# Performance work log

Measured on AMD Instinct MI355X. Metric: run time of the kernel, lower is better.

## Reference

```python
import jax, jax.numpy as jnp
import numpy as np

EMBED_DIM = 64
NUM_HEADS = 8
D_K = EMBED_DIM // NUM_HEADS  # 8
B, S = 8, 1024


def setup_inputs() -> dict:
    key = jax.random.key(0)
    ks = jax.random.split(key, 10)
    f32 = jnp.float32
    lim = 1.0 / np.sqrt(EMBED_DIM)
    def lin(k):
        kw, kb = jax.random.split(k)
        w = jax.random.uniform(kw, (EMBED_DIM, EMBED_DIM), f32, -lim, lim)
        b = jax.random.uniform(kb, (EMBED_DIM,), f32, -lim, lim)
        return w, b
    wq, bq = lin(ks[0])
    wk, bk = lin(ks[1])
    wv, bv = lin(ks[2])
    wo, bo = lin(ks[3])
    theta = jax.random.normal(ks[4], (EMBED_DIM,), f32)  # trainable RY angles, one per wire
    x = jax.random.normal(ks[5], (B, S, EMBED_DIM), f32)
    return {"x": x, "wq": wq, "bq": bq, "wk": wk, "bk": bk,
            "wv": wv, "bv": bv, "theta": theta, "wo": wo, "bo": bo}


def _quantum_map(t, theta):
    # Per-qubit circuit on |0>: RX(t_i) encode, RY(theta_i), <PauliZ_i>.
    # Product state => <Z_i> = cos(theta_i) * cos(t_i) exactly.
    return jnp.cos(theta) * jnp.cos(t.reshape(-1, EMBED_DIM))  # [N, E]


def reference(x, wq, bq, wk, bk, wv, bv, theta, wo, bo):
    # Linear QKV (torch nn.Linear: x @ W^T + b)
    q = x @ wq.T + bq
    k = x @ wk.T + bk
    v = x @ wv.T + bv
    # Quantum measurement map, flattened over batch*seq (as in the original)
    q_q = _quantum_map(q, theta)  # [N, E], N = B*S
    k_q = _quantum_map(k, theta)
    v_q = _quantum_map(v, theta)
    # Full flattened attention: [N, N] scores (original never reshapes back)
    scores = (q_q @ k_q.T) / jnp.sqrt(jnp.asarray(D_K, x.dtype))
    attn = jax.nn.softmax(scores, axis=-1)  # dropout is identity in eval
    out = attn @ v_q  # [N, E]
    return out @ wo.T + bo
```

## Files before the change

### kernel.cpp

```cpp
#include <hip/hip_runtime.h>
#include <hip/hip_bf16.h>

#define NQ 8192
#define DIM 64
#define SPLITS 8
#define QBLK 128
#define BN 64
#define KEYS_PER_SPLIT (NQ / SPLITS)
#define NTILES (KEYS_PER_SPLIT / BN)
#define SCALE 0.35355339059327373f

#define KSTR 72
#define PSTR 72

typedef short s8v __attribute__((ext_vector_type(8)));
typedef float f4v __attribute__((ext_vector_type(4)));

__device__ __forceinline__ float b2f(short s) {
  unsigned int u = ((unsigned int)(unsigned short)s) << 16;
  return __uint_as_float(u);
}
__device__ __forceinline__ short f2b(float f) {
  __hip_bfloat16 h = __float2bfloat16(f);
  return *reinterpret_cast<short*>(&h);
}

#define QROWS 16
__global__ __launch_bounds__(256) void qkv_kernel(
    const float* __restrict__ x,
    const float* __restrict__ wq, const float* __restrict__ bq,
    const float* __restrict__ wk, const float* __restrict__ bk,
    const float* __restrict__ wv, const float* __restrict__ bv,
    const float* __restrict__ theta,
    short* __restrict__ qq, short* __restrict__ kq, short* __restrict__ vq) {
  __shared__ float wsh[3][DIM][DIM + 1];
  __shared__ float xs[QROWS][DIM];
  int tid = threadIdx.x;
  for (int i = tid; i < 3 * DIM * (DIM / 4); i += 256) {
    int m = i / (DIM * DIM / 4);
    int rem = i % (DIM * DIM / 4);
    int r = rem / (DIM / 4);
    int c4 = (rem % (DIM / 4)) * 4;
    const float* src = (m == 0) ? wq : (m == 1) ? wk : wv;
    float4 v = *(const float4*)&src[r * DIM + c4];
    wsh[m][r][c4 + 0] = v.x; wsh[m][r][c4 + 1] = v.y;
    wsh[m][r][c4 + 2] = v.z; wsh[m][r][c4 + 3] = v.w;
  }
  int rowbase = blockIdx.x * QROWS;
  for (int i = tid; i < QROWS * (DIM / 4); i += 256) {
    int r = i / (DIM / 4), c4 = (i % (DIM / 4)) * 4;
    float4 v = *(const float4*)&x[(rowbase + r) * DIM + c4];
    xs[r][c4 + 0] = v.x; xs[r][c4 + 1] = v.y;
    xs[r][c4 + 2] = v.z; xs[r][c4 + 3] = v.w;
  }
  __syncthreads();
  int e = tid & 63, rg = tid >> 6;
  float ct = __cosf(theta[e]);
  float bqv = bq[e], bkv = bk[e], bvv = bv[e];
  for (int r = rg; r < QROWS; r += 4) {
    float aq = bqv, ak = bkv, av = bvv;
#pragma unroll
    for (int d = 0; d < DIM; ++d) {
      float xv = xs[r][d];
      aq += xv * wsh[0][e][d];
      ak += xv * wsh[1][e][d];
      av += xv * wsh[2][e][d];
    }
    int n = rowbase + r;
    qq[n * DIM + e] = f2b(ct * __cosf(aq));
    kq[n * DIM + e] = f2b(ct * __cosf(ak));
    vq[n * DIM + e] = f2b(ct * __cosf(av));
  }
}

__global__ __launch_bounds__(256, 2) void flash_kernel(
    const short* __restrict__ qq, const short* __restrict__ kq,
    const short* __restrict__ vq,
    float* __restrict__ pO, float* __restrict__ pL) {
  __shared__ __align__(16) short ksh[BN * KSTR];
  __shared__ __align__(16) short vsh[DIM * BN];
  __shared__ __align__(16) short psh[4][32 * PSTR];

  int tid = threadIdx.x;
  int wave = tid >> 6, lane = tid & 63;
  int l15 = lane & 15, quad = lane >> 4;
  int qblock = blockIdx.x >> 3, split = blockIdx.x & 7;
  int qbase = qblock * QBLK + wave * 32;

  s8v qf[2][2];
#pragma unroll
  for (int qt = 0; qt < 2; ++qt) {
    const short* qr = qq + (qbase + qt * 16 + l15) * DIM + quad * 8;
    qf[qt][0] = *(const s8v*)qr;
    qf[qt][1] = *(const s8v*)(qr + 32);
  }

  f4v o[2][4];
  float ls[2][4];
#pragma unroll
  for (int qt = 0; qt < 2; ++qt)
#pragma unroll
    for (int c = 0; c < 4; ++c) {
      o[qt][c] = (f4v){0.f, 0.f, 0.f, 0.f};
      ls[qt][c] = 0.f;
    }

  int kstart = split * KEYS_PER_SPLIT;
  for (int t = 0; t < NTILES; ++t) {
    int kbase = kstart + t * BN;
    __syncthreads();
    for (int i = tid; i < 512; i += 256) {
      int key = i >> 3, c8 = (i & 7) << 3;
      *(s8v*)&ksh[key * KSTR + c8] = *(const s8v*)&kq[(kbase + key) * DIM + c8];
    }
    for (int i = tid; i < 512; i += 256) {
      int key = i >> 3, d0 = (i & 7) << 3;
      s8v v = *(const s8v*)&vq[(kbase + key) * DIM + d0];
      int kb = key >> 3, ko = key & 7;
#pragma unroll
      for (int j = 0; j < 8; ++j) {
        int d = d0 + j;
        vsh[d * BN + (((kb ^ ((d ^ (d >> 3)) & 7)) << 3) + ko)] = v[j];
      }
    }
    __syncthreads();

    f4v s[2][4];
#pragma unroll
    for (int n = 0; n < 4; ++n) {
      s8v kf0 = *(const s8v*)&ksh[(n * 16 + l15) * KSTR + quad * 8];
      s8v kf1 = *(const s8v*)&ksh[(n * 16 + l15) * KSTR + 32 + quad * 8];
#pragma unroll
      for (int qt = 0; qt < 2; ++qt) {
        f4v acc = {0.f, 0.f, 0.f, 0.f};
        acc = __builtin_amdgcn_mfma_f32_16x16x32_bf16(qf[qt][0], kf0, acc, 0, 0, 0);
        acc = __builtin_amdgcn_mfma_f32_16x16x32_bf16(qf[qt][1], kf1, acc, 0, 0, 0);
        s[qt][n] = acc;
      }
    }

#pragma unroll
    for (int qt = 0; qt < 2; ++qt)
#pragma unroll
      for (int n = 0; n < 4; ++n)
#pragma unroll
        for (int r = 0; r < 4; ++r) {
          float p = __expf(s[qt][n][r] * SCALE);
          short pb = f2b(p);
          ls[qt][r] += b2f(pb);
          psh[wave][(qt * 16 + quad * 4 + r) * PSTR + n * 16 + l15] = pb;
        }
    __syncthreads();

    s8v pf[2][2];
#pragma unroll
    for (int qt = 0; qt < 2; ++qt) {
      pf[qt][0] = *(const s8v*)&psh[wave][(qt * 16 + l15) * PSTR + quad * 8];
      pf[qt][1] = *(const s8v*)&psh[wave][(qt * 16 + l15) * PSTR + 32 + quad * 8];
    }
#pragma unroll
    for (int c = 0; c < 4; ++c) {
      int d = c * 16 + l15;
      int sw = (d ^ (d >> 3)) & 7;
      s8v vf0 = *(const s8v*)&vsh[d * BN + ((quad ^ sw) << 3)];
      s8v vf1 = *(const s8v*)&vsh[d * BN + (((4 + quad) ^ sw) << 3)];
#pragma unroll
      for (int qt = 0; qt < 2; ++qt) {
        o[qt][c] = __builtin_amdgcn_mfma_f32_16x16x32_bf16(pf[qt][0], vf0, o[qt][c], 0, 0, 0);
        o[qt][c] = __builtin_amdgcn_mfma_f32_16x16x32_bf16(pf[qt][1], vf1, o[qt][c], 0, 0, 0);
      }
    }
  }

#pragma unroll
  for (int qt = 0; qt < 2; ++qt)
#pragma unroll
    for (int r = 0; r < 4; ++r) {
      float v = ls[qt][r];
      v += __shfl_xor(v, 1);
      v += __shfl_xor(v, 2);
      v += __shfl_xor(v, 4);
      v += __shfl_xor(v, 8);
      ls[qt][r] = v;
    }

#pragma unroll
  for (int qt = 0; qt < 2; ++qt)
#pragma unroll
    for (int r = 0; r < 4; ++r) {
      int q = qbase + qt * 16 + quad * 4 + r;
#pragma unroll
      for (int c = 0; c < 4; ++c)
        pO[((size_t)split * NQ + q) * DIM + c * 16 + l15] = o[qt][c][r];
      if (l15 == 0) pL[split * NQ + q] = ls[qt][r];
    }
}

#define MROWS 4
__global__ __launch_bounds__(256) void merge_kernel(
    const float* __restrict__ pO, const float* __restrict__ pL,
    const float* __restrict__ wo, const float* __restrict__ bo,
    float* __restrict__ out) {
  __shared__ float wsh[DIM][DIM + 1];
  __shared__ float att[MROWS][DIM];
  int tid = threadIdx.x;
  for (int i = tid; i < DIM * (DIM / 4); i += 256) {
    int r = i / (DIM / 4), c4 = (i % (DIM / 4)) * 4;
    float4 v = *(const float4*)&wo[r * DIM + c4];
    wsh[r][c4 + 0] = v.x; wsh[r][c4 + 1] = v.y;
    wsh[r][c4 + 2] = v.z; wsh[r][c4 + 3] = v.w;
  }
  int e = tid & 63, rg = tid >> 6;
  int q = blockIdx.x * MROWS + rg;
  float s = 0.f;
#pragma unroll
  for (int sp = 0; sp < SPLITS; ++sp) s += pO[((size_t)sp * NQ + q) * DIM + e];
  float l = 0.f;
#pragma unroll
  for (int sp = 0; sp < SPLITS; ++sp) l += pL[sp * NQ + q];
  att[rg][e] = s / l;
  __syncthreads();
  float acc = bo[e];
#pragma unroll
  for (int d = 0; d < DIM; ++d) acc += att[rg][d] * wsh[e][d];
  out[q * DIM + e] = acc;
}

extern "C" void kernel_launch(void* const* d_in, const int* in_sizes, int n_in,
                              void* d_out, int out_size, void* d_ws, size_t ws_size,
                              hipStream_t stream) {
  const float* x  = (const float*)d_in[0];
  const float* wq = (const float*)d_in[1];
  const float* bq = (const float*)d_in[2];
  const float* wk = (const float*)d_in[3];
  const float* bk = (const float*)d_in[4];
  const float* wv = (const float*)d_in[5];
  const float* bv = (const float*)d_in[6];
  const float* th = (const float*)d_in[7];
  const float* wo = (const float*)d_in[8];
  const float* bo = (const float*)d_in[9];

  char* ws = (char*)d_ws;
  short* qq = (short*)(ws);
  short* kq = (short*)(ws + (1u << 20));
  short* vq = (short*)(ws + (2u << 20));
  float* pO = (float*)(ws + (3u << 20));
  float* pL = (float*)(ws + (3u << 20) + (size_t)SPLITS * NQ * DIM * 4);

  hipLaunchKernelGGL(qkv_kernel, dim3(NQ / QROWS), dim3(256), 0, stream,
                     x, wq, bq, wk, bk, wv, bv, th, qq, kq, vq);
  hipLaunchKernelGGL(flash_kernel, dim3((NQ / QBLK) * SPLITS), dim3(256), 0, stream,
                     qq, kq, vq, pO, pL);
  hipLaunchKernelGGL(merge_kernel, dim3(NQ / MROWS), dim3(256), 0, stream,
                     pO, pL, wo, bo, (float*)d_out);
}
```

Measured before the change: 135.7 us.

## Keep P in registers via transposed QK MFMA, bf16 weights in QKV and merge

The flash kernel now computes S^T (K as the A operand) so each lane's accumulator outputs can feed directly as the A operand of a 16x16x16 bf16 MFMA for P·V. This removes the per-wave P shared-memory round trip and its extra barrier. V is stored transposed with a padded stride, exp2 with a prescaled constant replaces expf, and the row-sum reduction is simplified. The QKV and merge kernels convert weights and inputs to bf16 in shared memory with vectorised loads, and merge now handles 8 rows per block. The extra bf16 rounding of x and the weights may reduce accuracy.

```diff
diff --git a/kernel.cpp b/kernel.cpp
--- a/kernel.cpp
+++ b/kernel.cpp
@@ -9,11 +9,13 @@
 #define KEYS_PER_SPLIT (NQ / SPLITS)
 #define NTILES (KEYS_PER_SPLIT / BN)
 #define SCALE 0.35355339059327373f
+#define SC2   0.51012301920911057f
 
 #define KSTR 72
-#define PSTR 72
+#define VSTR 68
 
 typedef short s8v __attribute__((ext_vector_type(8)));
+typedef short s4v __attribute__((ext_vector_type(4)));
 typedef float f4v __attribute__((ext_vector_type(4)));
 
 __device__ __forceinline__ float b2f(short s) {
@@ -23,6 +25,17 @@
 __device__ __forceinline__ short f2b(float f) {
   __hip_bfloat16 h = __float2bfloat16(f);
   return *reinterpret_cast<short*>(&h);
+}
+
+__device__ __forceinline__ f4v mfma16(s4v a, s4v b, f4v c) {
+#if __has_builtin(__builtin_amdgcn_mfma_f32_16x16x16bf16_1k)
+  return __builtin_amdgcn_mfma_f32_16x16x16bf16_1k(a, b, c, 0, 0, 0);
+#else
+  f4v d;
+  asm volatile("v_mfma_f32_16x16x16_bf16 %0, %1, %2, %3"
+               : "=v"(d) : "v"(a), "v"(b), "v"(c));
+  return d;
+#endif
 }
 
 #define QROWS 16
@@ -33,25 +46,24 @@
     const float* __restrict__ wv, const float* __restrict__ bv,
     const float* __restrict__ theta,
     short* __restrict__ qq, short* __restrict__ kq, short* __restrict__ vq) {
-  __shared__ float wsh[3][DIM][DIM + 1];
-  __shared__ float xs[QROWS][DIM];
+  __shared__ __align__(16) short wsh[3][DIM][KSTR];
+  __shared__ __align__(16) short xsb[QROWS][DIM];
   int tid = threadIdx.x;
-  for (int i = tid; i < 3 * DIM * (DIM / 4); i += 256) {
-    int m = i / (DIM * DIM / 4);
-    int rem = i % (DIM * DIM / 4);
-    int r = rem / (DIM / 4);
-    int c4 = (rem % (DIM / 4)) * 4;
+  for (int i = tid; i < 3 * DIM * 16; i += 256) {
+    int m = i >> 10;
+    int rem = i & 1023;
+    int r = rem >> 4, c4 = (rem & 15) << 2;
     const float* src = (m == 0) ? wq : (m == 1) ? wk : wv;
-    float4 v = *(const float4*)&src[r * DIM + c4];
-    wsh[m][r][c4 + 0] = v.x; wsh[m][r][c4 + 1] = v.y;
-    wsh[m][r][c4 + 2] = v.z; wsh[m][r][c4 + 3] = v.w;
+    float4 w = *(const float4*)&src[r * DIM + c4];
+    s4v p = {f2b(w.x), f2b(w.y), f2b(w.z), f2b(w.w)};
+    *(s4v*)&wsh[m][r][c4] = p;
   }
   int rowbase = blockIdx.x * QROWS;
-  for (int i = tid; i < QROWS * (DIM / 4); i += 256) {
-    int r = i / (DIM / 4), c4 = (i % (DIM / 4)) * 4;
+  for (int i = tid; i < QROWS * 16; i += 256) {
+    int r = i >> 4, c4 = (i & 15) << 2;
     float4 v = *(const float4*)&x[(rowbase + r) * DIM + c4];
-    xs[r][c4 + 0] = v.x; xs[r][c4 + 1] = v.y;
-    xs[r][c4 + 2] = v.z; xs[r][c4 + 3] = v.w;
+    s4v p = {f2b(v.x), f2b(v.y), f2b(v.z), f2b(v.w)};
+    *(s4v*)&xsb[r][c4] = p;
   }
   __syncthreads();
   int e = tid & 63, rg = tid >> 6;
@@ -60,11 +72,18 @@
   for (int r = rg; r < QROWS; r += 4) {
     float aq = bqv, ak = bkv, av = bvv;
 #pragma unroll
-    for (int d = 0; d < DIM; ++d) {
-      float xv = xs[r][d];
-      aq += xv * wsh[0][e][d];
-      ak += xv * wsh[1][e][d];
-      av += xv * wsh[2][e][d];
+    for (int c8 = 0; c8 < 8; ++c8) {
+      s8v xv = *(const s8v*)&xsb[r][c8 * 8];
+      s8v w0 = *(const s8v*)&wsh[0][e][c8 * 8];
+      s8v w1 = *(const s8v*)&wsh[1][e][c8 * 8];
+      s8v w2 = *(const s8v*)&wsh[2][e][c8 * 8];
+#pragma unroll
+      for (int j = 0; j < 8; ++j) {
+        float xf = b2f(xv[j]);
+        aq += xf * b2f(w0[j]);
+        ak += xf * b2f(w1[j]);
+        av += xf * b2f(w2[j]);
+      }
     }
     int n = rowbase + r;
     qq[n * DIM + e] = f2b(ct * __cosf(aq));
@@ -73,13 +92,12 @@
   }
 }
 
-__global__ __launch_bounds__(256, 2) void flash_kernel(
+__global__ __launch_bounds__(256) void flash_kernel(
     const short* __restrict__ qq, const short* __restrict__ kq,
     const short* __restrict__ vq,
     float* __restrict__ pO, float* __restrict__ pL) {
   __shared__ __align__(16) short ksh[BN * KSTR];
-  __shared__ __align__(16) short vsh[DIM * BN];
-  __shared__ __align__(16) short psh[4][32 * PSTR];
+  __shared__ __align__(16) short vsh[DIM * VSTR];
 
   int tid = threadIdx.x;
   int wave = tid >> 6, lane = tid & 63;
@@ -96,14 +114,13 @@
   }
 
   f4v o[2][4];
-  float ls[2][4];
+  float ls[2] = {0.f, 0.f};
 #pragma unroll
   for (int qt = 0; qt < 2; ++qt)
 #pragma unroll
-    for (int c = 0; c < 4; ++c) {
-      o[qt][c] = (f4v){0.f, 0.f, 0.f, 0.f};
-      ls[qt][c] = 0.f;
-    }
+    for (int c = 0; c < 4; ++c) o[qt][c] = (f4v){0.f, 0.f, 0.f, 0.f};
+
+  int kp = tid & 31, dch = tid >> 5;
 
   int kstart = split * KEYS_PER_SPLIT;
   for (int t = 0; t < NTILES; ++t) {
@@ -113,117 +130,111 @@
       int key = i >> 3, c8 = (i & 7) << 3;
       *(s8v*)&ksh[key * KSTR + c8] = *(const s8v*)&kq[(kbase + key) * DIM + c8];
     }
-    for (int i = tid; i < 512; i += 256) {
-      int key = i >> 3, d0 = (i & 7) << 3;
-      s8v v = *(const s8v*)&vq[(kbase + key) * DIM + d0];
-      int kb = key >> 3, ko = key & 7;
+    {
+      s8v r0 = *(const s8v*)&vq[(kbase + 2 * kp) * DIM + (dch << 3)];
+      s8v r1 = *(const s8v*)&vq[(kbase + 2 * kp + 1) * DIM + (dch << 3)];
 #pragma unroll
       for (int j = 0; j < 8; ++j) {
-        int d = d0 + j;
-        vsh[d * BN + (((kb ^ ((d ^ (d >> 3)) & 7)) << 3) + ko)] = v[j];
+        int d = (dch << 3) + j;
+        int pk = (int)(unsigned short)r0[j] | ((int)(unsigned short)r1[j] << 16);
+        *(int*)&vsh[d * VSTR + 2 * kp] = pk;
       }
     }
     __syncthreads();
 
-    f4v s[2][4];
-#pragma unroll
-    for (int n = 0; n < 4; ++n) {
-      s8v kf0 = *(const s8v*)&ksh[(n * 16 + l15) * KSTR + quad * 8];
-      s8v kf1 = *(const s8v*)&ksh[(n * 16 + l15) * KSTR + 32 + quad * 8];
+#pragma unroll
+    for (int kt = 0; kt < 4; ++kt) {
+      const short* kr = &ksh[(kt * 16 + l15) * KSTR + quad * 8];
+      s8v kf0 = *(const s8v*)kr;
+      s8v kf1 = *(const s8v*)(kr + 32);
+      s4v pa[2];
 #pragma unroll
       for (int qt = 0; qt < 2; ++qt) {
-        f4v acc = {0.f, 0.f, 0.f, 0.f};
-        acc = __builtin_amdgcn_mfma_f32_16x16x32_bf16(qf[qt][0], kf0, acc, 0, 0, 0);
-        acc = __builtin_amdgcn_mfma_f32_16x16x32_bf16(qf[qt][1], kf1, acc, 0, 0, 0);
-        s[qt][n] = acc;
-      }
-    }
-
-#pragma unroll
-    for (int qt = 0; qt < 2; ++qt)
-#pragma unroll
-      for (int n = 0; n < 4; ++n)
+        f4v acc = (f4v){0.f, 0.f, 0.f, 0.f};
+        acc = __builtin_amdgcn_mfma_f32_16x16x32_bf16(kf0, qf[qt][0], acc, 0, 0, 0);
+        acc = __builtin_amdgcn_mfma_f32_16x16x32_bf16(kf1, qf[qt][1], acc, 0, 0, 0);
+        s4v a;
+        float sum = 0.f;
 #pragma unroll
         for (int r = 0; r < 4; ++r) {
-          float p = __expf(s[qt][n][r] * SCALE);
+          float p = exp2f(acc[r] * SC2);
           short pb = f2b(p);
-          ls[qt][r] += b2f(pb);
-          psh[wave][(qt * 16 + quad * 4 + r) * PSTR + n * 16 + l15] = pb;
+          a[r] = pb;
+          sum += b2f(pb);
         }
-    __syncthreads();
-
-    s8v pf[2][2];
-#pragma unroll
-    for (int qt = 0; qt < 2; ++qt) {
-      pf[qt][0] = *(const s8v*)&psh[wave][(qt * 16 + l15) * PSTR + quad * 8];
-      pf[qt][1] = *(const s8v*)&psh[wave][(qt * 16 + l15) * PSTR + 32 + quad * 8];
-    }
-#pragma unroll
-    for (int c = 0; c < 4; ++c) {
-      int d = c * 16 + l15;
-      int sw = (d ^ (d >> 3)) & 7;
-      s8v vf0 = *(const s8v*)&vsh[d * BN + ((quad ^ sw) << 3)];
-      s8v vf1 = *(const s8v*)&vsh[d * BN + (((4 + quad) ^ sw) << 3)];
-#pragma unroll
-      for (int qt = 0; qt < 2; ++qt) {
-        o[qt][c] = __builtin_amdgcn_mfma_f32_16x16x32_bf16(pf[qt][0], vf0, o[qt][c], 0, 0, 0);
-        o[qt][c] = __builtin_amdgcn_mfma_f32_16x16x32_bf16(pf[qt][1], vf1, o[qt][c], 0, 0, 0);
-      }
-    }
-  }
-
-#pragma unroll
-  for (int qt = 0; qt < 2; ++qt)
-#pragma unroll
-    for (int r = 0; r < 4; ++r) {
-      float v = ls[qt][r];
-      v += __shfl_xor(v, 1);
-      v += __shfl_xor(v, 2);
-      v += __shfl_xor(v, 4);
-      v += __shfl_xor(v, 8);
-      ls[qt][r] = v;
-    }
-
-#pragma unroll
-  for (int qt = 0; qt < 2; ++qt)
+        pa[qt] = a;
+        ls[qt] += sum;
+      }
+#pragma unroll
+      for (int c = 0; c < 4; ++c) {
+        s4v vf = *(const s4v*)&vsh[(c * 16 + l15) * VSTR + kt * 16 + quad * 4];
+#pragma unroll
+        for (int qt = 0; qt < 2; ++qt)
+          o[qt][c] = mfma16(pa[qt], vf, o[qt][c]);
+      }
+    }
+  }
+
+#pragma unroll
+  for (int qt = 0; qt < 2; ++qt) {
+    float v = ls[qt];
+    v += __shfl_xor(v, 16);
+    v += __shfl_xor(v, 32);
+    ls[qt] = v;
+  }
+
+#pragma unroll
+  for (int qt = 0; qt < 2; ++qt) {
 #pragma unroll
     for (int r = 0; r < 4; ++r) {
       int q = qbase + qt * 16 + quad * 4 + r;
 #pragma unroll
       for (int c = 0; c < 4; ++c)
         pO[((size_t)split * NQ + q) * DIM + c * 16 + l15] = o[qt][c][r];
-      if (l15 == 0) pL[split * NQ + q] = ls[qt][r];
-    }
-}
-
-#define MROWS 4
+    }
+    if (quad == 0) pL[split * NQ + qbase + qt * 16 + l15] = ls[qt];
+  }
+}
+
+#define MROWS 8
 __global__ __launch_bounds__(256) void merge_kernel(
     const float* __restrict__ pO, const float* __restrict__ pL,
     const float* __restrict__ wo, const float* __restrict__ bo,
     float* __restrict__ out) {
-  __shared__ float wsh[DIM][DIM + 1];
-  __shared__ float att[MROWS][DIM];
+  __shared__ __align__(16) short wsh[DIM][KSTR];
+  __shared__ __align__(16) float att[MROWS][DIM];
   int tid = threadIdx.x;
-  for (int i = tid; i < DIM * (DIM / 4); i += 256) {
-    int r = i / (DIM / 4), c4 = (i % (DIM / 4)) * 4;
-    float4 v = *(const float4*)&wo[r * DIM + c4];
-    wsh[r][c4 + 0] = v.x; wsh[r][c4 + 1] = v.y;
-    wsh[r][c4 + 2] = v.z; wsh[r][c4 + 3] = v.w;
+  for (int i = tid; i < DIM * 16; i += 256) {
+    int r = i >> 4, c4 = (i & 15) << 2;
+    float4 w = *(const float4*)&wo[r * DIM + c4];
+    s4v p = {f2b(w.x), f2b(w.y), f2b(w.z), f2b(w.w)};
+    *(s4v*)&wsh[r][c4] = p;
   }
   int e = tid & 63, rg = tid >> 6;
-  int q = blockIdx.x * MROWS + rg;
-  float s = 0.f;
-#pragma unroll
-  for (int sp = 0; sp < SPLITS; ++sp) s += pO[((size_t)sp * NQ + q) * DIM + e];
-  float l = 0.f;
-#pragma unroll
-  for (int sp = 0; sp < SPLITS; ++sp) l += pL[sp * NQ + q];
-  att[rg][e] = s / l;
+  int q0 = blockIdx.x * MROWS;
+  for (int rr = rg; rr < MROWS; rr += 4) {
+    int q = q0 + rr;
+    float s = 0.f, l = 0.f;
+#pragma unroll
+    for (int sp = 0; sp < SPLITS; ++sp) {
+      s += pO[((size_t)sp * NQ + q) * DIM + e];
+      l += pL[sp * NQ + q];
+    }
+    att[rr][e] = s / l;
+  }
   __syncthreads();
-  float acc = bo[e];
-#pragma unroll
-  for (int d = 0; d < DIM; ++d) acc += att[rg][d] * wsh[e][d];
-  out[q * DIM + e] = acc;
+  for (int rr = rg; rr < MROWS; rr += 4) {
+    float acc = bo[e];
+#pragma unroll
+    for (int c8 = 0; c8 < 8; ++c8) {
+      s8v w = *(const s8v*)&wsh[e][c8 * 8];
+      float4 a0 = *(const float4*)&att[rr][c8 * 8];
+      float4 a1 = *(const float4*)&att[rr][c8 * 8 + 4];
+      acc += a0.x * b2f(w[0]) + a0.y * b2f(w[1]) + a0.z * b2f(w[2]) + a0.w * b2f(w[3])
+           + a1.x * b2f(w[4]) + a1.y * b2f(w[5]) + a1.z * b2f(w[6]) + a1.w * b2f(w[7]);
+    }
+    out[(q0 + rr) * DIM + e] = acc;
+  }
 }
 
 extern "C" void kernel_launch(void* const* d_in, const int* in_sizes, int n_in,
```

After: 134.2 us. Within noise of the previous version (-1.1%).
